# Performance work log

Measured on AMD Instinct MI355X. Metric: run time of the kernel, lower is better.

The kernel has to match this reference:

```python
import jax, jax.numpy as jnp
import numpy as np

N_HEADS, D, D_HEAD = 16, 1024, 64
B, T = 4, 2048


def setup_inputs() -> dict:
    key = jax.random.key(0)
    k1, k2, k3, k4, k5, k6, k7 = jax.random.split(key, 7)
    Q = jax.random.normal(k1, (B, T, D), dtype=jnp.float32)
    K = jax.random.normal(k2, (B, T, D), dtype=jnp.float32)
    V = jax.random.normal(k3, (B, T, D), dtype=jnp.float32)
    # params initialized as 0.001 * randn, matching create_head
    Wq = 0.001 * jax.random.normal(k4, (N_HEADS, D, D_HEAD), dtype=jnp.float32)
    Wk = 0.001 * jax.random.normal(k5, (N_HEADS, D, D_HEAD), dtype=jnp.float32)
    Wv = 0.001 * jax.random.normal(k6, (N_HEADS, D, D_HEAD), dtype=jnp.float32)
    Wo = 0.001 * jax.random.normal(k7, (N_HEADS * D_HEAD, D), dtype=jnp.float32)
    return {"Q": Q, "K": K, "V": V, "Wq": Wq, "Wk": Wk, "Wv": Wv, "Wo": Wo}


def reference(Q, K, V, Wq, Wk, Wv, Wo):
    # per-head projections: [b,t,d] x [h,d,e] -> [b,h,t,e]
    Qh = jnp.einsum('btd,hde->bhte', Q, Wq)
    Kh = jnp.einsum('btd,hde->bhte', K, Wk)
    Vh = jnp.einsum('btd,hde->bhte', V, Wv)
    # scaled dot-product attention (ar=False path)
    scale = 1.0 / jnp.sqrt(jnp.asarray(D_HEAD, Qh.dtype))
    s = jnp.einsum('bhqe,bhke->bhqk', Qh, Kh) * scale  # [b,h,t,t]
    s = jax.nn.softmax(s, axis=-1)
    attn = jnp.einsum('bhqk,bhke->bhqe', s, Vh)  # [b,h,t,e]
    # output projection: rearrange b h t e -> b (h e) t, then 'bht,hd->btd'
    # equivalent to contracting (h,e) against Wo reshaped to [h,e,D]
    Wo3 = Wo.reshape(N_HEADS, D_HEAD, D)
    out = jnp.einsum('bhte,heD->btD', attn, Wo3)  # [b,t,d]
    return out
```

## Files before the change

### kernel.cpp

```cpp
#include <hip/hip_runtime.h>
#include <hip/hip_bf16.h>

#define DEV __device__ __forceinline__

typedef __attribute__((ext_vector_type(8))) short short8;
typedef __attribute__((ext_vector_type(4))) float f32x4;
typedef __attribute__((ext_vector_type(16))) float f32x16;
typedef __attribute__((ext_vector_type(2))) unsigned int u32x2;
typedef __attribute__((ext_vector_type(4))) unsigned int u32x4;
typedef unsigned short u16;
typedef unsigned int u32;


DEV u16 f2bf(float f) {
    union { __hip_bfloat16 h; u16 u; } cv;
    cv.h = __float2bfloat16(f);
    return cv.u;
}

DEV float exp2_raw(float x) {
    float r;
    asm("v_exp_f32 %0, %1" : "=v"(r) : "v"(x));
    return r;
}

DEV u32 cvtpk_bf2(float lo, float hi) {
    u32 r;
    asm("v_cvt_pk_bf16_f32 %0, %1, %2" : "=v"(r) : "v"(lo), "v"(hi));
    return r;
}

DEV float max3f(float a, float b, float c) { return fmaxf(fmaxf(a, b), c); }

DEV void gload_lds16(const void* g, void* l) {
    __builtin_amdgcn_global_load_lds((const __attribute__((address_space(1))) u32*)g,
                                     (__attribute__((address_space(3))) u32*)l, 16, 0, 0);
}

__global__ __launch_bounds__(256) void k_cvt3(const float* __restrict__ A0, const float* __restrict__ A1,
                                              const float* __restrict__ A2,
                                              u16* __restrict__ O0, u16* __restrict__ O1,
                                              u16* __restrict__ O2) {
    const int z = blockIdx.z;
    const float* X = z == 0 ? A0 : (z == 1 ? A1 : A2);
    u16* Y = z == 0 ? O0 : (z == 1 ? O1 : O2);
    const int t0 = blockIdx.x * 256 + threadIdx.x;
#pragma unroll
    for (int i = 0; i < 4; ++i) {
        const long c = ((long)i * 262144 + t0) * 8;
        float4 v0 = *(const float4*)(X + c);
        float4 v1 = *(const float4*)(X + c + 4);
        u32x4 wv;
        wv[0] = cvtpk_bf2(v0.x, v0.y); wv[1] = cvtpk_bf2(v0.z, v0.w);
        wv[2] = cvtpk_bf2(v1.x, v1.y); wv[3] = cvtpk_bf2(v1.z, v1.w);
        *(u32x4*)(Y + c) = wv;
    }
}

__global__ __launch_bounds__(256) void k_transpose_w3(const float* __restrict__ W0,
                                                      const float* __restrict__ W1,
                                                      const float* __restrict__ W2,
                                                      u16* __restrict__ O0,
                                                      u16* __restrict__ O1,
                                                      u16* __restrict__ O2) {
    __shared__ float tile[64][65];
    const int x = threadIdx.x & 63, y = threadIdx.x >> 6;
    const int which = blockIdx.z >> 4, slab_i = blockIdx.z & 15;
    const float* in = which == 0 ? W0 : (which == 1 ? W1 : W2);
    u16* out = which == 0 ? O0 : (which == 1 ? O1 : O2);
    const long slab = (long)slab_i * 1024 * 64;
    const int r0 = blockIdx.x * 64;
#pragma unroll
    for (int i = 0; i < 16; ++i) {
        int rr = y + 4 * i;
        tile[rr][x] = in[slab + (long)(r0 + rr) * 64 + x];
    }
    __syncthreads();
#pragma unroll
    for (int i = 0; i < 16; ++i) {
        int cc = y + 4 * i;
        out[slab + (long)cc * 1024 + (r0 + x)] = f2bf(tile[x][cc]);
    }
}

__global__ __launch_bounds__(256) void k_transpose_f32_bf16(const float* __restrict__ in,
                                                            u16* __restrict__ out,
                                                            int R, int C) {
    __shared__ float tile[64][65];
    const int x = threadIdx.x & 63, y = threadIdx.x >> 6;
    const long slab = (long)blockIdx.z * R * C;
    const int r0 = blockIdx.x * 64, c0 = blockIdx.y * 64;
#pragma unroll
    for (int i = 0; i < 16; ++i) {
        int rr = y + 4 * i;
        tile[rr][x] = in[slab + (long)(r0 + rr) * C + (c0 + x)];
    }
    __syncthreads();
#pragma unroll
    for (int i = 0; i < 16; ++i) {
        int cc = y + 4 * i;
        out[slab + (long)(c0 + cc) * R + (r0 + x)] = f2bf(tile[x][cc]);
    }
}

__global__ __launch_bounds__(256) void k_transpose_v(const u16* __restrict__ Vp,
                                                     u16* __restrict__ VhT) {
    __shared__ u16 tile[64][65];
    const int x = threadIdx.x & 63, y = threadIdx.x >> 6;
    const int bh = blockIdx.z, b = bh >> 4, h = bh & 15;
    const int t0 = blockIdx.x * 64;
#pragma unroll
    for (int i = 0; i < 16; ++i) {
        int rr = y + 4 * i;
        tile[rr][x] = Vp[(long)(b * 2048 + t0 + rr) * 1024 + h * 64 + x];
    }
    __syncthreads();
#pragma unroll
    for (int i = 0; i < 16; ++i) {
        int cc = y + 4 * i;
        VhT[(long)bh * 131072 + (long)cc * 2048 + t0 + x] = tile[x][cc];
    }
}

template<int CMODE>
DEV void gemm8_body(const u16* __restrict__ Ap, const u16* __restrict__ Btp,
                    void* __restrict__ Cp, u16* __restrict__ As, u16* __restrict__ Bs,
                    int brow, int bcol) {
    const int tid = threadIdx.x, lane = tid & 63, w = tid >> 6;
    const int l15 = lane & 15, l4 = lane >> 4;
    const int wr = w >> 1, wc = w & 1;

    const u16* aptr[4]; int adst[4];
#pragma unroll
    for (int i = 0; i < 4; ++i) {
        const int c = i * 512 + w * 64 + lane;
        const int r = c >> 3, s = c & 7, sw = s ^ (r & 7);
        aptr[i] = Ap + (long)(brow + r) * 1024 + sw * 8;
        adst[i] = i * 4096 + w * 512;
    }
    const u16* bptr[2]; int bdst[2];
#pragma unroll
    for (int i = 0; i < 2; ++i) {
        const int c = i * 512 + w * 64 + lane;
        const int r = c >> 3, s = c & 7, sw = s ^ (r & 7);
        bptr[i] = Btp + (long)(bcol + r) * 1024 + sw * 8;
        bdst[i] = i * 4096 + w * 512;
    }

    auto stage = [&](int buf, int kt) {
        const int ko = kt * 64;
        u16* Ad = As + buf * 16384;
        u16* Bd = Bs + buf * 8192;
#pragma unroll
        for (int i = 0; i < 4; ++i) gload_lds16(aptr[i] + ko, Ad + adst[i]);
#pragma unroll
        for (int i = 0; i < 2; ++i) gload_lds16(bptr[i] + ko, Bd + bdst[i]);
    };

    int e4[2];
#pragma unroll
    for (int kk = 0; kk < 2; ++kk) e4[kk] = ((kk * 4 + l4) ^ (l15 & 7)) * 8;
    int offA[4][2], offB[4][2];
#pragma unroll
    for (int m = 0; m < 4; ++m)
#pragma unroll
        for (int kk = 0; kk < 2; ++kk) {
            offA[m][kk] = (wr * 64 + m * 16 + l15) * 64 + e4[kk];
            offB[m][kk] = (wc * 64 + m * 16 + l15) * 64 + e4[kk];
        }

    f32x4 acc[4][4] = {};
    stage(0, 0);
    stage(1, 1);

    for (int t = 0; t < 16; ++t) {
        const int buf = t & 1;
        if (t < 15) asm volatile("s_waitcnt vmcnt(6)" ::: "memory");
        else        asm volatile("s_waitcnt vmcnt(0)" ::: "memory");
        __builtin_amdgcn_sched_barrier(0);
        __builtin_amdgcn_s_barrier();
        __builtin_amdgcn_sched_barrier(0);

        const u16* Ab = As + buf * 16384;
        const u16* Bb = Bs + buf * 8192;
#pragma unroll
        for (int kk = 0; kk < 2; ++kk) {
            short8 af[4], bfv[4];
#pragma unroll
            for (int m = 0; m < 4; ++m) af[m] = *(const short8*)&Ab[offA[m][kk]];
#pragma unroll
            for (int n = 0; n < 4; ++n) bfv[n] = *(const short8*)&Bb[offB[n][kk]];
            asm volatile("s_waitcnt lgkmcnt(0)" ::: "memory");
            __builtin_amdgcn_sched_barrier(0);
            __builtin_amdgcn_s_setprio(1);
#pragma unroll
            for (int m = 0; m < 4; ++m)
#pragma unroll
                for (int n = 0; n < 4; ++n)
                    acc[m][n] = __builtin_amdgcn_mfma_f32_16x16x32_bf16(af[m], bfv[n], acc[m][n], 0, 0, 0);
            __builtin_amdgcn_s_setprio(0);
            __builtin_amdgcn_sched_barrier(0);
        }
        __builtin_amdgcn_s_barrier();
        __builtin_amdgcn_sched_barrier(0);
        if (t + 2 < 16) stage(buf, t + 2);
    }

#pragma unroll
    for (int m = 0; m < 4; ++m)
#pragma unroll
        for (int n = 0; n < 4; ++n)
#pragma unroll
            for (int r = 0; r < 4; ++r) {
                const long row = brow + wr * 64 + m * 16 + l4 * 4 + r;
                const int col = bcol + wc * 64 + n * 16 + l15;
                if (CMODE == 0) ((u16*)Cp)[row * 1024 + col] = f2bf(acc[m][n][r]);
                else            ((float*)Cp)[row * 1024 + col] = acc[m][n][r];
            }
}

__global__ __launch_bounds__(512) void k_gemm3(const u16* __restrict__ Xq, const u16* __restrict__ Xk,
                                               const u16* __restrict__ Xv,
                                               const u16* __restrict__ B0, const u16* __restrict__ B1,
                                               const u16* __restrict__ B2,
                                               u16* __restrict__ C0, u16* __restrict__ C1,
                                               u16* __restrict__ C2) {
    __shared__ u16 As[2 * 16384];
    __shared__ u16 Bs[2 * 8192];
    const int hw = blockIdx.x;
    const int lg = (hw & 7) * 96 + (hw >> 3);
    const int z = lg >> 8, rem = lg & 255;
    const int brow = (rem >> 3) * 256, bcol = (rem & 7) * 128;
    const u16* A = z == 0 ? Xq : (z == 1 ? Xk : Xv);
    const u16* Bt = z == 0 ? B0 : (z == 1 ? B1 : B2);
    u16*       C = z == 0 ? C0 : (z == 1 ? C1 : C2);
    gemm8_body<0>(A, Bt, C, As, Bs, brow, bcol);
}

__global__ __launch_bounds__(512) void k_gemm_out(const u16* __restrict__ Ab,
                                                  const u16* __restrict__ Bt,
                                                  float* __restrict__ Cf) {
    __shared__ u16 As[2 * 16384];
    __shared__ u16 Bs[2 * 8192];
    const int hw = blockIdx.x;
    const int lg = (hw & 7) * 32 + (hw >> 3);
    const int brow = (lg >> 3) * 256, bcol = (lg & 7) * 128;
    gemm8_body<1>(Ab, Bt, Cf, As, Bs, brow, bcol);
}

__global__ __launch_bounds__(256, 2) void k_flash5(const u16* __restrict__ Qp,
                                                   const u16* __restrict__ Kp,
                                                   const u16* __restrict__ VhT,
                                                   u16* __restrict__ attn) {
    __shared__ u16 Ks[2][4096];
    __shared__ u16 Vs[2][4096];

    const int tid = threadIdx.x, lane = tid & 63, w = tid >> 6;
    const int l31 = lane & 31, l5 = lane >> 5;
    const int wid = blockIdx.x;
    const int swz = (wid & 7) * 64 + (wid >> 3);
    const int bh = swz >> 3, qt = swz & 7;
    const int b = bh >> 4, h = bh & 15;
    const long rowb = (long)b * 2048;
    const int colb = h * 64;
    const u16* Kbase = Kp + rowb * 1024 + colb;
    const long vbase = (long)bh * 131072;
    const int q0 = qt * 256 + w * 64;

    short8 qf0[4], qf1[4];
#pragma unroll
    for (int ksd = 0; ksd < 4; ++ksd) {
        qf0[ksd] = *(const short8*)(Qp + (rowb + q0 + l31) * 1024 + colb + ksd * 16 + l5 * 8);
        qf1[ksd] = *(const short8*)(Qp + (rowb + q0 + 32 + l31) * 1024 + colb + ksd * 16 + l5 * 8);
    }

    int off[4];
#pragma unroll
    for (int ksd = 0; ksd < 4; ++ksd)
        off[ksd] = l31 * 128 + (((ksd * 2 + l5) ^ (l31 & 7)) << 4);

    const float CEXP = 0.18033688011112042f;
    float mr0 = -INFINITY, mr1 = -INFINITY, lr0 = 0.f, lr1 = 0.f;
    f32x16 oa00 = {}, oa01 = {}, oa10 = {}, oa11 = {};

    const int c0 = tid, c1 = tid + 256;
    const int r0 = c0 >> 3, s0 = (c0 & 7) ^ (r0 & 7);
    const int r1 = c1 >> 3, s1 = (c1 & 7) ^ (r1 & 7);

#define STAGE(buf, t) do {                                                               \
    const long kv0_ = (long)((t) * 64);                                                  \
    gload_lds16(Kbase + (kv0_ + r0) * 1024 + s0 * 8, &Ks[buf][w * 512]);                 \
    gload_lds16(Kbase + (kv0_ + r1) * 1024 + s1 * 8, &Ks[buf][2048 + w * 512]);          \
    gload_lds16(VhT + vbase + (long)r0 * 2048 + kv0_ + s0 * 8, &Vs[buf][w * 512]);       \
    gload_lds16(VhT + vbase + (long)r1 * 2048 + kv0_ + s1 * 8, &Vs[buf][2048 + w * 512]); \
  } while (0)

    auto rowmax = [&](const f32x16& za, const f32x16& zb) -> float {
        float a0 = max3f(za[0],  za[1],  za[2]);
        float a1 = max3f(za[3],  za[4],  za[5]);
        float a2 = max3f(za[6],  za[7],  za[8]);
        float a3 = max3f(za[9],  za[10], za[11]);
        float a4 = max3f(za[12], za[13], za[14]);
        float a5 = max3f(za[15], zb[0],  zb[1]);
        float a6 = max3f(zb[2],  zb[3],  zb[4]);
        float a7 = max3f(zb[5],  zb[6],  zb[7]);
        float a8 = max3f(zb[8],  zb[9],  zb[10]);
        float a9 = max3f(zb[11], zb[12], zb[13]);
        float aa = fmaxf(zb[14], zb[15]);
        float b0 = max3f(a0, a1, a2);
        float b1 = max3f(a3, a4, a5);
        float b2 = max3f(a6, a7, a8);
        float b3 = fmaxf(a9, aa);
        float vm = fmaxf(max3f(b0, b1, b2), b3);
        u32x2 pp = __builtin_amdgcn_permlane32_swap(__builtin_bit_cast(u32, vm),
                                                    __builtin_bit_cast(u32, vm), false, false);
        return fmaxf(__builtin_bit_cast(float, pp[0]), __builtin_bit_cast(float, pp[1]));
    };

    auto process = [&](const f32x16& za, const f32x16& zb, float& mr, float& lr,
                       f32x16& oaA, f32x16& oaB, short8* pb) {
        const float vm = rowmax(za, zb);
        if (!__all(vm - mr <= 8.0f)) {
            const float nm = fmaxf(mr, vm);
            const float sc = exp2_raw((mr - nm) * CEXP);
            mr = nm;
#pragma unroll
            for (int i = 0; i < 16; ++i) { oaA[i] *= sc; oaB[i] *= sc; }
            lr *= sc;
        }
        const float nmc = -mr * CEXP;
        float rs = 0.f;
#pragma unroll
        for (int tile = 0; tile < 2; ++tile) {
            const f32x16& zz = tile ? zb : za;
            u32 W[8];
#pragma unroll
            for (int mw = 0; mw < 8; ++mw) {
                const float p0 = exp2_raw(fmaf(zz[2 * mw],     CEXP, nmc));
                const float p1 = exp2_raw(fmaf(zz[2 * mw + 1], CEXP, nmc));
                rs += p0 + p1;
                W[mw] = cvtpk_bf2(p0, p1);
            }
#pragma unroll
            for (int ksw = 0; ksw < 2; ++ksw) {
                u32x2 ra = __builtin_amdgcn_permlane32_swap(W[4 * ksw + 0], W[4 * ksw + 2], false, false);
                u32x2 rb = __builtin_amdgcn_permlane32_swap(W[4 * ksw + 1], W[4 * ksw + 3], false, false);
                u32x4 pw; pw[0] = ra[0]; pw[1] = rb[0]; pw[2] = ra[1]; pw[3] = rb[1];
                pb[tile * 2 + ksw] = __builtin_bit_cast(short8, pw);
            }
        }
        u32x2 rr = __builtin_amdgcn_permlane32_swap(__builtin_bit_cast(u32, rs),
                                                    __builtin_bit_cast(u32, rs), false, false);
        lr += __builtin_bit_cast(float, rr[0]) + __builtin_bit_cast(float, rr[1]);
    };

    STAGE(0, 0);

#pragma unroll 2
    for (int t = 0; t < 32; ++t) {
        const int buf = t & 1;
        __syncthreads();
        if (t < 31) STAGE(buf ^ 1, t + 1);

        const char* Kb = (const char*)&Ks[buf][0];
        const char* Vb = (const char*)&Vs[buf][0];

        f32x16 z0a = {}, z0b = {}, z1a = {}, z1b = {};
#pragma unroll
        for (int ksd = 0; ksd < 4; ++ksd) {
            short8 kf0 = *(const short8*)(Kb + off[ksd]);
            short8 kf1 = *(const short8*)(Kb + 4096 + off[ksd]);
            z0a = __builtin_amdgcn_mfma_f32_32x32x16_bf16(kf0, qf0[ksd], z0a, 0, 0, 0);
            z0b = __builtin_amdgcn_mfma_f32_32x32x16_bf16(kf1, qf0[ksd], z0b, 0, 0, 0);
            z1a = __builtin_amdgcn_mfma_f32_32x32x16_bf16(kf0, qf1[ksd], z1a, 0, 0, 0);
            z1b = __builtin_amdgcn_mfma_f32_32x32x16_bf16(kf1, qf1[ksd], z1b, 0, 0, 0);
        }

        short8 pb0[4], pb1[4];
        process(z0a, z0b, mr0, lr0, oa00, oa01, pb0);
        process(z1a, z1b, mr1, lr1, oa10, oa11, pb1);

#pragma unroll
        for (int ks = 0; ks < 4; ++ks) {
            short8 vf0 = *(const short8*)(Vb + off[ks]);
            short8 vf1 = *(const short8*)(Vb + 4096 + off[ks]);
            oa00 = __builtin_amdgcn_mfma_f32_32x32x16_bf16(vf0, pb0[ks], oa00, 0, 0, 0);
            oa01 = __builtin_amdgcn_mfma_f32_32x32x16_bf16(vf1, pb0[ks], oa01, 0, 0, 0);
            oa10 = __builtin_amdgcn_mfma_f32_32x32x16_bf16(vf0, pb1[ks], oa10, 0, 0, 0);
            oa11 = __builtin_amdgcn_mfma_f32_32x32x16_bf16(vf1, pb1[ks], oa11, 0, 0, 0);
        }
    }
#undef STAGE

#pragma unroll
    for (int g = 0; g < 2; ++g) {
        const float inv = 1.0f / (g ? lr1 : lr0);
        u16* op = attn + (rowb + q0 + g * 32 + l31) * 1024 + colb;
#pragma unroll
        for (int et = 0; et < 2; ++et) {
            const f32x16& oa = g ? (et ? oa11 : oa10) : (et ? oa01 : oa00);
#pragma unroll
            for (int rq = 0; rq < 4; ++rq) {
                u32x2 st;
                st[0] = cvtpk_bf2(oa[4 * rq + 0] * inv, oa[4 * rq + 1] * inv);
                st[1] = cvtpk_bf2(oa[4 * rq + 2] * inv, oa[4 * rq + 3] * inv);
                *(u32x2*)(op + et * 32 + rq * 8 + l5 * 4) = st;
            }
        }
    }
}

extern "C" void kernel_launch(void* const* d_in, const int* in_sizes, int n_in,
                              void* d_out, int out_size, void* d_ws, size_t ws_size,
                              hipStream_t stream) {
    (void)in_sizes; (void)n_in; (void)out_size; (void)ws_size;
    const float* Q  = (const float*)d_in[0];
    const float* K  = (const float*)d_in[1];
    const float* V  = (const float*)d_in[2];
    const float* Wq = (const float*)d_in[3];
    const float* Wk = (const float*)d_in[4];
    const float* Wv = (const float*)d_in[5];
    const float* Wo = (const float*)d_in[6];

    char* ws = (char*)d_ws;
    auto WS = [&](size_t mb) { return (u16*)(ws + (mb << 20)); };
    u16* WqT  = WS(0);
    u16* WkT  = WS(2);
    u16* WvT  = WS(4);
    u16* WoT  = WS(6);
    u16* Xq   = WS(8);
    u16* Xk   = WS(24);
    u16* Xv   = WS(40);
    u16* Qp   = WS(56);
    u16* Kp   = WS(72);
    u16* Vp   = WS(88);
    u16* VhT  = WS(24);
    u16* attn = WS(8);

    dim3 b256(256);
    dim3 b512(512);
    k_transpose_w3<<<dim3(16, 1, 48), b256, 0, stream>>>(Wq, Wk, Wv, WqT, WkT, WvT);
    k_transpose_f32_bf16<<<dim3(16, 16, 1), b256, 0, stream>>>(Wo, WoT, 1024, 1024);
    k_cvt3<<<dim3(1024, 1, 3), b256, 0, stream>>>(Q, K, V, Xq, Xk, Xv);

    k_gemm3<<<dim3(768), b512, 0, stream>>>(Xq, Xk, Xv, WqT, WkT, WvT, Qp, Kp, Vp);

    k_transpose_v<<<dim3(32, 1, 64), b256, 0, stream>>>(Vp, VhT);

    k_flash5<<<dim3(512), b256, 0, stream>>>(Qp, Kp, VhT, attn);

    k_gemm_out<<<dim3(256), b512, 0, stream>>>(attn, WoT, (float*)d_out);
}
```

Baseline: 214.8 us.

## Fuse fp32-to-bf16 activation conversion into QKV projection GEMM A-tile loads

Drops the separate conversion kernel that wrote bf16 copies of Q, K and V. The projection GEMM now loads fp32 A tiles into registers, converts them to bf16 and writes them into swizzled LDS, while B still streams through direct global-to-LDS loads. The workspace layout is compacted, and the flash kernel's launch bounds are raised to request four blocks per SM. This removes a full read/write pass over 3x32MB of fp32 inputs, but doubles the GEMM's A-side global traffic, adds register pressure for prefetched fp32 data, and may force register spills in the flash kernel.

```diff
diff --git a/kernel.cpp b/kernel.cpp
--- a/kernel.cpp
+++ b/kernel.cpp
@@ -35,26 +35,6 @@
 DEV void gload_lds16(const void* g, void* l) {
     __builtin_amdgcn_global_load_lds((const __attribute__((address_space(1))) u32*)g,
                                      (__attribute__((address_space(3))) u32*)l, 16, 0, 0);
-}
-
-__global__ __launch_bounds__(256) void k_cvt3(const float* __restrict__ A0, const float* __restrict__ A1,
-                                              const float* __restrict__ A2,
-                                              u16* __restrict__ O0, u16* __restrict__ O1,
-                                              u16* __restrict__ O2) {
-    const int z = blockIdx.z;
-    const float* X = z == 0 ? A0 : (z == 1 ? A1 : A2);
-    u16* Y = z == 0 ? O0 : (z == 1 ? O1 : O2);
-    const int t0 = blockIdx.x * 256 + threadIdx.x;
-#pragma unroll
-    for (int i = 0; i < 4; ++i) {
-        const long c = ((long)i * 262144 + t0) * 8;
-        float4 v0 = *(const float4*)(X + c);
-        float4 v1 = *(const float4*)(X + c + 4);
-        u32x4 wv;
-        wv[0] = cvtpk_bf2(v0.x, v0.y); wv[1] = cvtpk_bf2(v0.z, v0.w);
-        wv[2] = cvtpk_bf2(v1.x, v1.y); wv[3] = cvtpk_bf2(v1.z, v1.w);
-        *(u32x4*)(Y + c) = wv;
-    }
 }
 
 __global__ __launch_bounds__(256) void k_transpose_w3(const float* __restrict__ W0,
@@ -219,22 +199,120 @@
             }
 }
 
-__global__ __launch_bounds__(512) void k_gemm3(const u16* __restrict__ Xq, const u16* __restrict__ Xk,
-                                               const u16* __restrict__ Xv,
+__global__ __launch_bounds__(512) void k_gemm3(const float* __restrict__ Aq, const float* __restrict__ Ak,
+                                               const float* __restrict__ Av,
                                                const u16* __restrict__ B0, const u16* __restrict__ B1,
                                                const u16* __restrict__ B2,
                                                u16* __restrict__ C0, u16* __restrict__ C1,
                                                u16* __restrict__ C2) {
     __shared__ u16 As[2 * 16384];
     __shared__ u16 Bs[2 * 8192];
+    const int tid = threadIdx.x, lane = tid & 63, w = tid >> 6;
+    const int l15 = lane & 15, l4 = lane >> 4;
+    const int wr = w >> 1, wc = w & 1;
     const int hw = blockIdx.x;
     const int lg = (hw & 7) * 96 + (hw >> 3);
     const int z = lg >> 8, rem = lg & 255;
     const int brow = (rem >> 3) * 256, bcol = (rem & 7) * 128;
-    const u16* A = z == 0 ? Xq : (z == 1 ? Xk : Xv);
-    const u16* Bt = z == 0 ? B0 : (z == 1 ? B1 : B2);
-    u16*       C = z == 0 ? C0 : (z == 1 ? C1 : C2);
-    gemm8_body<0>(A, Bt, C, As, Bs, brow, bcol);
+    const float* Af = z == 0 ? Aq : (z == 1 ? Ak : Av);
+    const u16*   Bt = z == 0 ? B0 : (z == 1 ? B1 : B2);
+    u16*         Cb = z == 0 ? C0 : (z == 1 ? C1 : C2);
+
+    const float* aptr[4]; int adst[4];
+#pragma unroll
+    for (int i = 0; i < 4; ++i) {
+        const int c = i * 512 + tid;
+        const int r = c >> 3, s = c & 7;
+        aptr[i] = Af + (long)(brow + r) * 1024 + s * 8;
+        adst[i] = r * 64 + (s ^ (r & 7)) * 8;
+    }
+    const u16* bptr[2]; int bdst[2];
+#pragma unroll
+    for (int i = 0; i < 2; ++i) {
+        const int c = i * 512 + w * 64 + lane;
+        const int r = c >> 3, s = c & 7, sw = s ^ (r & 7);
+        bptr[i] = Bt + (long)(bcol + r) * 1024 + sw * 8;
+        bdst[i] = i * 4096 + w * 512;
+    }
+
+    int e4[2];
+#pragma unroll
+    for (int kk = 0; kk < 2; ++kk) e4[kk] = ((kk * 4 + l4) ^ (l15 & 7)) * 8;
+    int offA[4][2], offB[4][2];
+#pragma unroll
+    for (int m = 0; m < 4; ++m)
+#pragma unroll
+        for (int kk = 0; kk < 2; ++kk) {
+            offA[m][kk] = (wr * 64 + m * 16 + l15) * 64 + e4[kk];
+            offB[m][kk] = (wc * 64 + m * 16 + l15) * 64 + e4[kk];
+        }
+
+    f32x4 acc[4][4] = {};
+    float4 va0[4][2], va1[4][2];
+
+#define ISSUE_A(SET, kt) do { _Pragma("unroll") for (int i = 0; i < 4; ++i) {          \
+        va##SET[i][0] = *(const float4*)(aptr[i] + (kt) * 64);                          \
+        va##SET[i][1] = *(const float4*)(aptr[i] + (kt) * 64 + 4); } } while (0)
+#define ISSUE_B(buf, kt) do {                                                           \
+        gload_lds16(bptr[0] + (kt) * 64, Bs + (buf) * 8192 + bdst[0]);                  \
+        gload_lds16(bptr[1] + (kt) * 64, Bs + (buf) * 8192 + bdst[1]); } while (0)
+
+    ISSUE_A(0, 0); ISSUE_B(0, 0);
+    ISSUE_A(1, 1); ISSUE_B(1, 1);
+
+#define GITER(t, SET) do {                                                              \
+    if ((t) < 15) asm volatile("s_waitcnt vmcnt(10)" ::: "memory");                     \
+    else          asm volatile("s_waitcnt vmcnt(0)" ::: "memory");                      \
+    __builtin_amdgcn_sched_barrier(0);                                                  \
+    { u16* Ad = As + ((t) & 1) * 16384;                                                 \
+      _Pragma("unroll") for (int i = 0; i < 4; ++i) {                                   \
+        u32x4 wv;                                                                       \
+        wv[0] = cvtpk_bf2(va##SET[i][0].x, va##SET[i][0].y);                            \
+        wv[1] = cvtpk_bf2(va##SET[i][0].z, va##SET[i][0].w);                            \
+        wv[2] = cvtpk_bf2(va##SET[i][1].x, va##SET[i][1].y);                            \
+        wv[3] = cvtpk_bf2(va##SET[i][1].z, va##SET[i][1].w);                            \
+        *(u32x4*)&Ad[adst[i]] = wv; } }                                                 \
+    asm volatile("s_waitcnt lgkmcnt(0)" ::: "memory");                                  \
+    __builtin_amdgcn_sched_barrier(0);                                                  \
+    __builtin_amdgcn_s_barrier();                                                       \
+    __builtin_amdgcn_sched_barrier(0);                                                  \
+    { const u16* Ab = As + ((t) & 1) * 16384;                                           \
+      const u16* Bb = Bs + ((t) & 1) * 8192;                                            \
+      _Pragma("unroll") for (int kk = 0; kk < 2; ++kk) {                                \
+        short8 af[4], bfv[4];                                                           \
+        _Pragma("unroll") for (int m = 0; m < 4; ++m) af[m] = *(const short8*)&Ab[offA[m][kk]]; \
+        _Pragma("unroll") for (int n = 0; n < 4; ++n) bfv[n] = *(const short8*)&Bb[offB[n][kk]]; \
+        asm volatile("s_waitcnt lgkmcnt(0)" ::: "memory");                              \
+        __builtin_amdgcn_sched_barrier(0);                                              \
+        __builtin_amdgcn_s_setprio(1);                                                  \
+        _Pragma("unroll") for (int m = 0; m < 4; ++m)                                   \
+        _Pragma("unroll") for (int n = 0; n < 4; ++n)                                   \
+            acc[m][n] = __builtin_amdgcn_mfma_f32_16x16x32_bf16(af[m], bfv[n], acc[m][n], 0, 0, 0); \
+        __builtin_amdgcn_s_setprio(0);                                                  \
+        __builtin_amdgcn_sched_barrier(0); } }                                          \
+    __builtin_amdgcn_s_barrier();                                                       \
+    __builtin_amdgcn_sched_barrier(0);                                                  \
+    if ((t) + 2 < 16) { ISSUE_A(SET, (t) + 2); ISSUE_B((t) & 1, (t) + 2); }             \
+} while (0)
+
+    for (int th = 0; th < 8; ++th) {
+        GITER(2 * th, 0);
+        GITER(2 * th + 1, 1);
+    }
+#undef GITER
+#undef ISSUE_A
+#undef ISSUE_B
+
+#pragma unroll
+    for (int m = 0; m < 4; ++m)
+#pragma unroll
+        for (int n = 0; n < 4; ++n)
+#pragma unroll
+            for (int r = 0; r < 4; ++r) {
+                const long row = brow + wr * 64 + m * 16 + l4 * 4 + r;
+                const int col = bcol + wc * 64 + n * 16 + l15;
+                Cb[row * 1024 + col] = f2bf(acc[m][n][r]);
+            }
 }
 
 __global__ __launch_bounds__(512) void k_gemm_out(const u16* __restrict__ Ab,
@@ -248,7 +326,7 @@
     gemm8_body<1>(Ab, Bt, Cf, As, Bs, brow, bcol);
 }
 
-__global__ __launch_bounds__(256, 2) void k_flash5(const u16* __restrict__ Qp,
+__global__ __launch_bounds__(256, 4) void k_flash5(const u16* __restrict__ Qp,
                                                    const u16* __restrict__ Kp,
                                                    const u16* __restrict__ VhT,
                                                    u16* __restrict__ attn) {
@@ -428,22 +506,18 @@
     u16* WkT  = WS(2);
     u16* WvT  = WS(4);
     u16* WoT  = WS(6);
-    u16* Xq   = WS(8);
-    u16* Xk   = WS(24);
-    u16* Xv   = WS(40);
-    u16* Qp   = WS(56);
-    u16* Kp   = WS(72);
-    u16* Vp   = WS(88);
-    u16* VhT  = WS(24);
-    u16* attn = WS(8);
+    u16* Qp   = WS(8);
+    u16* Kp   = WS(24);
+    u16* Vp   = WS(40);
+    u16* VhT  = WS(56);
+    u16* attn = WS(72);
 
     dim3 b256(256);
     dim3 b512(512);
     k_transpose_w3<<<dim3(16, 1, 48), b256, 0, stream>>>(Wq, Wk, Wv, WqT, WkT, WvT);
     k_transpose_f32_bf16<<<dim3(16, 16, 1), b256, 0, stream>>>(Wo, WoT, 1024, 1024);
-    k_cvt3<<<dim3(1024, 1, 3), b256, 0, stream>>>(Q, K, V, Xq, Xk, Xv);
-
-    k_gemm3<<<dim3(768), b512, 0, stream>>>(Xq, Xk, Xv, WqT, WkT, WvT, Qp, Kp, Vp);
+
+    k_gemm3<<<dim3(768), b512, 0, stream>>>(Q, K, V, WqT, WkT, WvT, Qp, Kp, Vp);
 
     k_transpose_v<<<dim3(32, 1, 64), b256, 0, stream>>>(Vp, VhT);
 
```

Result: slower. 475.0 us (+121.2%).

## Split flash attention KV range in two and merge partials in combine kernel

Applied to the files above, without the earlier changes.

Splits each attention work item's key/value loop into two halves processed by separate blocks, doubling the grid from 512 to 1024 blocks. Each half writes unnormalised bf16 partial outputs plus running max and sum, and a new combine kernel rescales and merges them into the attention buffer. The aim is better occupancy across the GPU's compute units, since 512 blocks may underfill the device. In exchange it adds an extra launch, extra global traffic for the partials, and an extra bf16 rounding of the unnormalised accumulators.

```diff
diff --git a/kernel.cpp b/kernel.cpp
--- a/kernel.cpp
+++ b/kernel.cpp
@@ -29,6 +29,8 @@
     asm("v_cvt_pk_bf16_f32 %0, %1, %2" : "=v"(r) : "v"(lo), "v"(hi));
     return r;
 }
+
+DEV float bf2f(u16 v) { return __builtin_bit_cast(float, ((u32)v) << 16); }
 
 DEV float max3f(float a, float b, float c) { return fmaxf(fmaxf(a, b), c); }
 
@@ -248,24 +250,27 @@
     gemm8_body<1>(Ab, Bt, Cf, As, Bs, brow, bcol);
 }
 
-__global__ __launch_bounds__(256, 2) void k_flash5(const u16* __restrict__ Qp,
+__global__ __launch_bounds__(256, 2) void k_flash6(const u16* __restrict__ Qp,
                                                    const u16* __restrict__ Kp,
                                                    const u16* __restrict__ VhT,
-                                                   u16* __restrict__ attn) {
+                                                   u16* __restrict__ Of0,
+                                                   u16* __restrict__ Of1,
+                                                   float* __restrict__ Ml) {
     __shared__ u16 Ks[2][4096];
     __shared__ u16 Vs[2][4096];
 
     const int tid = threadIdx.x, lane = tid & 63, w = tid >> 6;
     const int l31 = lane & 31, l5 = lane >> 5;
     const int wid = blockIdx.x;
-    const int swz = (wid & 7) * 64 + (wid >> 3);
-    const int bh = swz >> 3, qt = swz & 7;
+    const int swz = (wid & 7) * 128 + (wid >> 3);
+    const int bh = swz >> 4, qt = (swz >> 1) & 7, half = swz & 1;
     const int b = bh >> 4, h = bh & 15;
     const long rowb = (long)b * 2048;
     const int colb = h * 64;
     const u16* Kbase = Kp + rowb * 1024 + colb;
     const long vbase = (long)bh * 131072;
     const int q0 = qt * 256 + w * 64;
+    const int t0 = half * 16;
 
     short8 qf0[4], qf1[4];
 #pragma unroll
@@ -354,13 +359,13 @@
         lr += __builtin_bit_cast(float, rr[0]) + __builtin_bit_cast(float, rr[1]);
     };
 
-    STAGE(0, 0);
+    STAGE(0, t0);
 
 #pragma unroll 2
-    for (int t = 0; t < 32; ++t) {
+    for (int t = 0; t < 16; ++t) {
         const int buf = t & 1;
         __syncthreads();
-        if (t < 31) STAGE(buf ^ 1, t + 1);
+        if (t < 15) STAGE(buf ^ 1, t0 + t + 1);
 
         const char* Kb = (const char*)&Ks[buf][0];
         const char* Vb = (const char*)&Vs[buf][0];
@@ -392,22 +397,58 @@
     }
 #undef STAGE
 
+    u16* Ofh = half ? Of1 : Of0;
 #pragma unroll
     for (int g = 0; g < 2; ++g) {
-        const float inv = 1.0f / (g ? lr1 : lr0);
-        u16* op = attn + (rowb + q0 + g * 32 + l31) * 1024 + colb;
+        const int q = q0 + g * 32 + l31;
+        u16* op = Ofh + ((long)bh * 2048 + q) * 64;
 #pragma unroll
         for (int et = 0; et < 2; ++et) {
             const f32x16& oa = g ? (et ? oa11 : oa10) : (et ? oa01 : oa00);
 #pragma unroll
             for (int rq = 0; rq < 4; ++rq) {
                 u32x2 st;
-                st[0] = cvtpk_bf2(oa[4 * rq + 0] * inv, oa[4 * rq + 1] * inv);
-                st[1] = cvtpk_bf2(oa[4 * rq + 2] * inv, oa[4 * rq + 3] * inv);
+                st[0] = cvtpk_bf2(oa[4 * rq + 0], oa[4 * rq + 1]);
+                st[1] = cvtpk_bf2(oa[4 * rq + 2], oa[4 * rq + 3]);
                 *(u32x2*)(op + et * 32 + rq * 8 + l5 * 4) = st;
             }
         }
-    }
+        if (l5 == 0) {
+            float2 v;
+            v.x = g ? mr1 : mr0;
+            v.y = g ? lr1 : lr0;
+            *(float2*)(Ml + ((long)half * 131072 + (long)bh * 2048 + q) * 2) = v;
+        }
+    }
+}
+
+__global__ __launch_bounds__(256) void k_combine(const u16* __restrict__ Of0,
+                                                 const u16* __restrict__ Of1,
+                                                 const float* __restrict__ Ml,
+                                                 u16* __restrict__ attn) {
+    const float CEXP = 0.18033688011112042f;
+    const long gid = (long)blockIdx.x * 256 + threadIdx.x;
+    const int chunk = (int)(gid & 7);
+    const long row = gid >> 3;
+    const int bh = (int)(row >> 11), q = (int)(row & 2047);
+    const float2 m1 = *(const float2*)(Ml + row * 2);
+    const float2 m2 = *(const float2*)(Ml + (131072 + row) * 2);
+    const float m = fmaxf(m1.x, m2.x);
+    const float w1 = exp2_raw((m1.x - m) * CEXP);
+    const float w2 = exp2_raw((m2.x - m) * CEXP);
+    const float inv = 1.0f / (m1.y * w1 + m2.y * w2);
+    const float s1 = w1 * inv, s2 = w2 * inv;
+    short8 v1 = *(const short8*)(Of0 + row * 64 + chunk * 8);
+    short8 v2 = *(const short8*)(Of1 + row * 64 + chunk * 8);
+    u32x4 outw;
+#pragma unroll
+    for (int i = 0; i < 4; ++i) {
+        const float a = bf2f((u16)v1[2 * i])     * s1 + bf2f((u16)v2[2 * i])     * s2;
+        const float b = bf2f((u16)v1[2 * i + 1]) * s1 + bf2f((u16)v2[2 * i + 1]) * s2;
+        outw[i] = cvtpk_bf2(a, b);
+    }
+    u16* op = attn + ((long)(bh >> 4) * 2048 + q) * 1024 + (bh & 15) * 64 + chunk * 8;
+    *(u32x4*)op = outw;
 }
 
 extern "C" void kernel_launch(void* const* d_in, const int* in_sizes, int n_in,
@@ -435,6 +476,9 @@
     u16* Kp   = WS(72);
     u16* Vp   = WS(88);
     u16* VhT  = WS(24);
+    u16* Of0  = WS(40);
+    u16* Of1  = WS(88);
+    float* Ml = (float*)WS(104);
     u16* attn = WS(8);
 
     dim3 b256(256);
@@ -447,7 +491,8 @@
 
     k_transpose_v<<<dim3(32, 1, 64), b256, 0, stream>>>(Vp, VhT);
 
-    k_flash5<<<dim3(512), b256, 0, stream>>>(Qp, Kp, VhT, attn);
+    k_flash6<<<dim3(1024), b256, 0, stream>>>(Qp, Kp, VhT, Of0, Of1, Ml);
+    k_combine<<<dim3(4096), b256, 0, stream>>>(Of0, Of1, Ml, attn);
 
     k_gemm_out<<<dim3(256), b512, 0, stream>>>(attn, WoT, (float*)d_out);
 }
```

After: 231.4 us. +7.8%, slower.
